# Kernel optimization log

Measured on AMD Instinct MI355X. Metric: run time of the kernel, lower is better.

Reference implementation:

```python
import jax, jax.numpy as jnp
import numpy as np

N = 200_000        # nodes
E = 2_000_000      # edges (before self loops)
D = 128            # emb_dim
L = 5              # num_layer
NUM_ATOM = 120     # num_atom_type
NUM_CHI = 3        # num_chirality_tag
NUM_BOND = 6       # num_bond_type
NUM_DIR = 3        # num_bond_direction
EPS = 1e-5


def setup_inputs() -> dict:
    key = jax.random.key(0)
    ks = jax.random.split(key, 12)
    s = 0.1
    return {
        "x": jax.random.randint(ks[0], (N, 2), 0, 3, dtype=jnp.int64) if jax.config.jax_enable_x64 else jax.random.randint(ks[0], (N, 2), 0, 3, dtype=jnp.int32),
        "edge_index": jax.random.randint(ks[1], (2, E), 0, N, dtype=jnp.int32),
        "edge_attr": jax.random.randint(ks[2], (E, 2), 0, 3, dtype=jnp.int32),
        "x_emb1": jax.random.normal(ks[3], (NUM_ATOM, D), jnp.float32) * s,
        "x_emb2": jax.random.normal(ks[4], (NUM_CHI, D), jnp.float32) * s,
        "edge_emb1": jax.random.normal(ks[5], (L, NUM_BOND, D), jnp.float32) * s,
        "edge_emb2": jax.random.normal(ks[6], (L, NUM_DIR, D), jnp.float32) * s,
        "w1": jax.random.normal(ks[7], (L, D, 2 * D), jnp.float32) * s,
        "b1": jnp.zeros((L, 2 * D), jnp.float32),
        "w2": jax.random.normal(ks[8], (L, 2 * D, D), jnp.float32) * s,
        "b2": jnp.zeros((L, D), jnp.float32),
        "bn_gamma": jnp.ones((L, D), jnp.float32),
        "bn_beta": jnp.zeros((L, D), jnp.float32),
    }


def reference(x, edge_index, edge_attr, x_emb1, x_emb2, edge_emb1, edge_emb2,
              w1, b1, w2, b2, bn_gamma, bn_beta):
    # node features: atom-type emb + chirality emb
    h = x_emb1[x[:, 0]] + x_emb2[x[:, 1]]                     # [N, D]

    # add self loops; self-loop edge_attr = [4, 0]
    loop = jnp.arange(N, dtype=edge_index.dtype)
    src = jnp.concatenate([edge_index[0], loop])              # [E+N]
    dst = jnp.concatenate([edge_index[1], loop])              # [E+N]
    ea0 = jnp.concatenate([edge_attr[:, 0], jnp.full((N,), 4, edge_attr.dtype)])
    ea1 = jnp.concatenate([edge_attr[:, 1], jnp.zeros((N,), edge_attr.dtype)])

    for l in range(L):
        e_emb = edge_emb1[l][ea0] + edge_emb2[l][ea1]         # [E+N, D]
        msg = h[src] + e_emb                                  # gather + add
        agg = jax.ops.segment_sum(msg, dst, num_segments=N)   # scatter-add
        hid = jax.nn.relu(agg @ w1[l] + b1[l])                # [N, 2D]
        hn = hid @ w2[l] + b2[l]                              # [N, D]
        # BatchNorm1d (training mode, biased variance)
        mean = hn.mean(axis=0)
        var = jnp.mean((hn - mean) ** 2, axis=0)
        hn = bn_gamma[l] * (hn - mean) * jax.lax.rsqrt(var + EPS) + bn_beta[l]
        if l < L - 1:
            hn = jax.nn.relu(hn)
        h = hn
    return h
```

## Files before the change

kernel.cpp:

```cpp
#include <hip/hip_runtime.h>

#define NN 200000
#define NPAD 200192
#define NE 2000000
#define DD 128
#define EPSF 1e-5f

typedef short short4v __attribute__((ext_vector_type(4)));
typedef short short8v __attribute__((ext_vector_type(8)));
typedef float f32x4 __attribute__((ext_vector_type(4)));
typedef unsigned long long u64;

__device__ __forceinline__ ushort f2bf(float f) {
  uint u = __float_as_uint(f);
  uint r = u + 0x7fff + ((u >> 16) & 1);
  return (ushort)(r >> 16);
}
__device__ __forceinline__ float bf2f(ushort u) { return __uint_as_float(((uint)u) << 16); }
__device__ __forceinline__ float bflo(uint v) { return __uint_as_float(v << 16); }
__device__ __forceinline__ float bfhi(uint v) { return __uint_as_float(v & 0xffff0000u); }
__device__ __forceinline__ uint packbf(float a, float b) {
  return (uint)f2bf(a) | ((uint)f2bf(b) << 16);
}

__device__ __forceinline__ short8v ldfrag(const ushort* p) {
  short4v lo = *(const short4v*)p;
  short4v hi = *(const short4v*)(p + 16);
  short8v r;
  r[0] = lo[0]; r[1] = lo[1]; r[2] = lo[2]; r[3] = lo[3];
  r[4] = hi[0]; r[5] = hi[1]; r[6] = hi[2]; r[7] = hi[3];
  return r;
}

__global__ __launch_bounds__(256) void k_init(const int* __restrict__ x,
    const float* __restrict__ e1, const float* __restrict__ e2,
    uint* __restrict__ h) {
  int t = blockIdx.x * 256 + threadIdx.x;
  if (t >= NN * 64) return;
  int node = t >> 6, cp = (t & 63) << 1;
  int a = x[2 * node], b = x[2 * node + 1];
  float2 va = *(const float2*)(e1 + (size_t)a * DD + cp);
  float2 vb = *(const float2*)(e2 + (size_t)b * DD + cp);
  h[t] = packbf(va.x + vb.x, va.y + vb.y);
}

__global__ __launch_bounds__(256) void k_cvtw(const float* __restrict__ w,
    ushort* __restrict__ wt, int K, int Nc) {
  int t = blockIdx.x * 256 + threadIdx.x;
  if (t >= 5 * K * Nc) return;
  int per = K * Nc;
  int l = t / per, r0 = t % per;
  int j = r0 & 7, lane = (r0 >> 3) & 63, idx = r0 >> 9;
  int KB = K >> 5;
  int kb = idx % KB, ct = idx / KB;
  int lr = lane & 15, qq = lane >> 4;
  int n = ct * 16 + lr;
  int k = kb * 32 + qq * 4 + (j & 3) + ((j >> 2) << 4);
  wt[t] = f2bf(w[(size_t)l * per + (size_t)k * Nc + n]);
}

__global__ __launch_bounds__(256) void k_hist(const int* __restrict__ ei,
    const int* __restrict__ ea, u64* __restrict__ hist8) {
  int e = blockIdx.x * 256 + threadIdx.x;
  if (e >= NE) return;
  int d = ei[NE + e];
  int a0 = ea[2 * e];
  int a1 = ea[2 * e + 1];
  u64 v = (1ull << (a0 * 10)) | (1ull << (30 + a1 * 10));
  atomicAdd(&hist8[(size_t)(blockIdx.x & 7) * NN + d], v);
}

__global__ __launch_bounds__(256) void k_scan1(const u64* __restrict__ hist8,
    u64* __restrict__ histsum, int* __restrict__ off, int* __restrict__ bsum) {
  __shared__ int sh[256];
  int i = blockIdx.x * 256 + threadIdx.x;
  int v = 0;
  if (i < NN) {
    u64 s = 0;
#pragma unroll
    for (int cc = 0; cc < 8; ++cc) s += hist8[(size_t)cc * NN + i];
    histsum[i] = s;
    v = (int)((s & 1023) + ((s >> 10) & 1023) + ((s >> 20) & 1023));
  }
  sh[threadIdx.x] = v;
  __syncthreads();
  for (int d = 1; d < 256; d <<= 1) {
    int xv = 0;
    if (threadIdx.x >= d) xv = sh[threadIdx.x - d];
    __syncthreads();
    if (threadIdx.x >= d) sh[threadIdx.x] += xv;
    __syncthreads();
  }
  if (i < NN) off[i] = sh[threadIdx.x] - v;
  if (threadIdx.x == 255) bsum[blockIdx.x] = sh[255];
}

__global__ __launch_bounds__(1024) void k_scan2(const int* __restrict__ bsum,
    int* __restrict__ boff, int nb) {
  __shared__ int sh[1024];
  int t = threadIdx.x;
  int v = (t < nb) ? bsum[t] : 0;
  sh[t] = v;
  __syncthreads();
  for (int d = 1; d < 1024; d <<= 1) {
    int xv = 0;
    if (t >= d) xv = sh[t - d];
    __syncthreads();
    if (t >= d) sh[t] += xv;
    __syncthreads();
  }
  if (t < nb) boff[t] = sh[t] - v;
}

__global__ __launch_bounds__(256) void k_scan3(int* __restrict__ off,
    const int* __restrict__ boff, int* __restrict__ cursor) {
  int i = blockIdx.x * 256 + threadIdx.x;
  if (i < NN) {
    int o = off[i] + boff[i >> 8];
    off[i] = o;
    cursor[i] = o;
  }
  if (i == 0) off[NN] = NE;
}

__global__ __launch_bounds__(256) void k_scatter(const int* __restrict__ ei,
    int* __restrict__ cursor, int* __restrict__ csr_src) {
  int e = blockIdx.x * 256 + threadIdx.x;
  if (e >= NE) return;
  int d = ei[NE + e];
  int p = atomicAdd(&cursor[d], 1);
  csr_src[p] = ei[e];
}

__global__ __launch_bounds__(256) void k_agg(const uint* __restrict__ h,
    uint* __restrict__ agghi, uint* __restrict__ agglo,
    const int* __restrict__ off, const int* __restrict__ src,
    const u64* __restrict__ hist,
    const float* __restrict__ E1, const float* __restrict__ E2) {
  int lane = threadIdx.x & 63;
  int node = blockIdx.x * 4 + (threadIdx.x >> 6);
  int qq = lane >> 4;
  int c = lane & 15;
  float a[8];
#pragma unroll
  for (int j = 0; j < 8; ++j) a[j] = 0.f;
  int beg = off[node], end = off[node + 1];
  int deg = end - beg;
  for (int base = 0; base < deg; base += 64) {
    int nrem = min(deg - base, 64);
    int myidx = 0;
    if (lane < nrem) myidx = src[beg + base + lane];
    int niter = (nrem + 3) >> 2;
    for (int m = 0; m < niter; m += 4) {
      int sl0 = qq + 4 * m;
      int sl1 = sl0 + 4, sl2 = sl0 + 8, sl3 = sl0 + 12;
      int s0 = __shfl(myidx, min(sl0, nrem - 1));
      int s1 = __shfl(myidx, min(sl1, nrem - 1));
      int s2 = __shfl(myidx, min(sl2, nrem - 1));
      int s3 = __shfl(myidx, min(sl3, nrem - 1));
      uint4 v0 = *(const uint4*)(h + (size_t)s0 * 64 + c * 4);
      if (sl0 < nrem) {
        a[0] += bflo(v0.x); a[1] += bfhi(v0.x);
        a[2] += bflo(v0.y); a[3] += bfhi(v0.y);
        a[4] += bflo(v0.z); a[5] += bfhi(v0.z);
        a[6] += bflo(v0.w); a[7] += bfhi(v0.w);
      }
      if (m + 1 < niter) {
        uint4 v1 = *(const uint4*)(h + (size_t)s1 * 64 + c * 4);
        if (sl1 < nrem) {
          a[0] += bflo(v1.x); a[1] += bfhi(v1.x);
          a[2] += bflo(v1.y); a[3] += bfhi(v1.y);
          a[4] += bflo(v1.z); a[5] += bfhi(v1.z);
          a[6] += bflo(v1.w); a[7] += bfhi(v1.w);
        }
      }
      if (m + 2 < niter) {
        uint4 v2 = *(const uint4*)(h + (size_t)s2 * 64 + c * 4);
        if (sl2 < nrem) {
          a[0] += bflo(v2.x); a[1] += bfhi(v2.x);
          a[2] += bflo(v2.y); a[3] += bfhi(v2.y);
          a[4] += bflo(v2.z); a[5] += bfhi(v2.z);
          a[6] += bflo(v2.w); a[7] += bfhi(v2.w);
        }
      }
      if (m + 3 < niter) {
        uint4 v3 = *(const uint4*)(h + (size_t)s3 * 64 + c * 4);
        if (sl3 < nrem) {
          a[0] += bflo(v3.x); a[1] += bfhi(v3.x);
          a[2] += bflo(v3.y); a[3] += bfhi(v3.y);
          a[4] += bflo(v3.z); a[5] += bfhi(v3.z);
          a[6] += bflo(v3.w); a[7] += bfhi(v3.w);
        }
      }
    }
  }
#pragma unroll
  for (int j = 0; j < 8; ++j) {
    a[j] += __shfl_xor(a[j], 16);
    a[j] += __shfl_xor(a[j], 32);
  }
  if (lane < 16) {
    uint4 sv = *(const uint4*)(h + (size_t)node * 64 + c * 4);
    a[0] += bflo(sv.x); a[1] += bfhi(sv.x);
    a[2] += bflo(sv.y); a[3] += bfhi(sv.y);
    a[4] += bflo(sv.z); a[5] += bfhi(sv.z);
    a[6] += bflo(sv.w); a[7] += bfhi(sv.w);
    u64 hv = hist[node];
    float cnt[7] = {
      (float)(int)(hv & 1023),
      (float)(int)((hv >> 10) & 1023),
      (float)(int)((hv >> 20) & 1023),
      1.f,
      (float)(int)((hv >> 30) & 1023) + 1.f,
      (float)(int)((hv >> 40) & 1023),
      (float)(int)((hv >> 50) & 1023)
    };
    const float* rows[7] = {E1, E1 + DD, E1 + 2 * DD, E1 + 4 * DD,
                            E2, E2 + DD, E2 + 2 * DD};
#pragma unroll
    for (int q = 0; q < 7; ++q) {
      f32x4 e0 = *(const f32x4*)(rows[q] + c * 8);
      f32x4 e1v = *(const f32x4*)(rows[q] + c * 8 + 4);
#pragma unroll
      for (int j = 0; j < 4; ++j) { a[j] += cnt[q] * e0[j]; a[4 + j] += cnt[q] * e1v[j]; }
    }
    uint4 hi4, lo4;
    {
      ushort hA, hB;
      hA = f2bf(a[0]); hB = f2bf(a[1]);
      hi4.x = (uint)hA | ((uint)hB << 16);
      lo4.x = (uint)f2bf(a[0] - bf2f(hA)) | ((uint)f2bf(a[1] - bf2f(hB)) << 16);
      hA = f2bf(a[2]); hB = f2bf(a[3]);
      hi4.y = (uint)hA | ((uint)hB << 16);
      lo4.y = (uint)f2bf(a[2] - bf2f(hA)) | ((uint)f2bf(a[3] - bf2f(hB)) << 16);
      hA = f2bf(a[4]); hB = f2bf(a[5]);
      hi4.z = (uint)hA | ((uint)hB << 16);
      lo4.z = (uint)f2bf(a[4] - bf2f(hA)) | ((uint)f2bf(a[5] - bf2f(hB)) << 16);
      hA = f2bf(a[6]); hB = f2bf(a[7]);
      hi4.w = (uint)hA | ((uint)hB << 16);
      lo4.w = (uint)f2bf(a[6] - bf2f(hA)) | ((uint)f2bf(a[7] - bf2f(hB)) << 16);
    }
    *(uint4*)(agghi + (size_t)node * 64 + c * 4) = hi4;
    *(uint4*)(agglo + (size_t)node * 64 + c * 4) = lo4;
  }
}

__global__ __launch_bounds__(512, 1) void k_mlp(
    const ushort* __restrict__ agghi, const ushort* __restrict__ agglo,
    const ushort* __restrict__ w1,
    const float* __restrict__ b1,
    const ushort* __restrict__ w2,
    const float* __restrict__ b2, float* __restrict__ hn,
    float* __restrict__ bnsums) {
  __shared__ uint4 smem4[8192];
  __shared__ float sstat[256];
  const ushort* sw1 = (const ushort*)smem4;
  const ushort* sw2 = (const ushort*)(smem4 + 4096);
  int t = threadIdx.x;
  int lane = t & 63;
  int wid = t >> 6;
  int nb = blockIdx.x * 256 + wid * 32;
  int lr = lane & 15, qq = lane >> 4;

  if (t < 256) sstat[t] = 0.f;

  short8v afh[2][4], afl[2][4];
#pragma unroll
  for (int g = 0; g < 2; ++g) {
    const ushort* ph = agghi + (size_t)(nb + g * 16 + lr) * 128 + qq * 4;
    const ushort* pl = agglo + (size_t)(nb + g * 16 + lr) * 128 + qq * 4;
#pragma unroll
    for (int kb = 0; kb < 4; ++kb) {
      afh[g][kb] = ldfrag(ph + kb * 32);
      afl[g][kb] = ldfrag(pl + kb * 32);
    }
  }

  {
    const uint4* g1 = (const uint4*)w1;
    const uint4* g2 = (const uint4*)w2;
#pragma unroll
    for (int i = 0; i < 8; ++i) smem4[i * 512 + t] = g1[i * 512 + t];
#pragma unroll
    for (int i = 0; i < 8; ++i) smem4[4096 + i * 512 + t] = g2[i * 512 + t];
  }
  __syncthreads();

  f32x4 acc2[2][8];
#pragma unroll
  for (int g = 0; g < 2; ++g)
#pragma unroll
    for (int ct = 0; ct < 8; ++ct) acc2[g][ct] = (f32x4){0.f, 0.f, 0.f, 0.f};

#pragma unroll
  for (int ph = 0; ph < 4; ++ph) {
    f32x4 acc1[2][4];
#pragma unroll
    for (int g = 0; g < 2; ++g)
#pragma unroll
      for (int ct = 0; ct < 4; ++ct) acc1[g][ct] = (f32x4){0.f, 0.f, 0.f, 0.f};
#pragma unroll
    for (int ct = 0; ct < 4; ++ct) {
      int gct = ph * 4 + ct;
#pragma unroll
      for (int kb = 0; kb < 4; ++kb) {
        short8v wf = *(const short8v*)(sw1 + ((gct * 4 + kb) * 64 + lane) * 8);
        acc1[0][ct] = __builtin_amdgcn_mfma_f32_16x16x32_bf16(wf, afh[0][kb], acc1[0][ct], 0, 0, 0);
        acc1[0][ct] = __builtin_amdgcn_mfma_f32_16x16x32_bf16(wf, afl[0][kb], acc1[0][ct], 0, 0, 0);
        acc1[1][ct] = __builtin_amdgcn_mfma_f32_16x16x32_bf16(wf, afh[1][kb], acc1[1][ct], 0, 0, 0);
        acc1[1][ct] = __builtin_amdgcn_mfma_f32_16x16x32_bf16(wf, afl[1][kb], acc1[1][ct], 0, 0, 0);
      }
    }
    short8v hfh[2][2], hfl[2][2];
#pragma unroll
    for (int i = 0; i < 2; ++i) {
      f32x4 ba = *(const f32x4*)(b1 + (ph * 4 + 2 * i) * 16 + qq * 4);
      f32x4 bb = *(const f32x4*)(b1 + (ph * 4 + 2 * i + 1) * 16 + qq * 4);
#pragma unroll
      for (int g = 0; g < 2; ++g) {
        short8v hh, hl;
#pragma unroll
        for (int r = 0; r < 4; ++r) {
          float va = fmaxf(acc1[g][2 * i][r] + ba[r], 0.f);
          float vb = fmaxf(acc1[g][2 * i + 1][r] + bb[r], 0.f);
          ushort ha = f2bf(va), hb = f2bf(vb);
          hh[r] = (short)ha; hh[4 + r] = (short)hb;
          hl[r] = (short)f2bf(va - bf2f(ha));
          hl[4 + r] = (short)f2bf(vb - bf2f(hb));
        }
        hfh[g][i] = hh; hfl[g][i] = hl;
      }
    }
#pragma unroll
    for (int ct = 0; ct < 8; ++ct) {
#pragma unroll
      for (int i = 0; i < 2; ++i) {
        int kb2 = ph * 2 + i;
        short8v wf = *(const short8v*)(sw2 + ((ct * 8 + kb2) * 64 + lane) * 8);
        acc2[0][ct] = __builtin_amdgcn_mfma_f32_16x16x32_bf16(wf, hfh[0][i], acc2[0][ct], 0, 0, 0);
        acc2[0][ct] = __builtin_amdgcn_mfma_f32_16x16x32_bf16(wf, hfl[0][i], acc2[0][ct], 0, 0, 0);
        acc2[1][ct] = __builtin_amdgcn_mfma_f32_16x16x32_bf16(wf, hfh[1][i], acc2[1][ct], 0, 0, 0);
        acc2[1][ct] = __builtin_amdgcn_mfma_f32_16x16x32_bf16(wf, hfl[1][i], acc2[1][ct], 0, 0, 0);
      }
    }
  }

  int n0 = nb + lr, n1 = nb + 16 + lr;
  float m0 = (n0 < NN) ? 1.f : 0.f;
  float m1 = (n1 < NN) ? 1.f : 0.f;
#pragma unroll
  for (int ct = 0; ct < 8; ++ct) {
    f32x4 bb = *(const f32x4*)(b2 + ct * 16 + qq * 4);
    f32x4 o0, o1;
#pragma unroll
    for (int r = 0; r < 4; ++r) {
      o0[r] = acc2[0][ct][r] + bb[r];
      o1[r] = acc2[1][ct][r] + bb[r];
    }
#pragma unroll
    for (int r = 0; r < 4; ++r) {
      float s = m0 * o0[r] + m1 * o1[r];
      float q = m0 * o0[r] * o0[r] + m1 * o1[r] * o1[r];
      s += __shfl_xor(s, 1); q += __shfl_xor(q, 1);
      s += __shfl_xor(s, 2); q += __shfl_xor(q, 2);
      s += __shfl_xor(s, 4); q += __shfl_xor(q, 4);
      s += __shfl_xor(s, 8); q += __shfl_xor(q, 8);
      if (lr == 0) {
        int col = ct * 16 + qq * 4 + r;
        atomicAdd(&sstat[col], s);
        atomicAdd(&sstat[128 + col], q);
      }
    }
    if (n0 < NN) *(f32x4*)(hn + (size_t)n0 * DD + ct * 16 + qq * 4) = o0;
    if (n1 < NN) *(f32x4*)(hn + (size_t)n1 * DD + ct * 16 + qq * 4) = o1;
  }
  __syncthreads();
  if (t < 256) atomicAdd(&bnsums[t], sstat[t]);
}

__global__ __launch_bounds__(256) void k_bnapply(const float* __restrict__ hn,
    const float* __restrict__ sums, const float* __restrict__ gamma,
    const float* __restrict__ beta, uint* __restrict__ hout,
    float* __restrict__ fout, int final_layer) {
  int t = blockIdx.x * 256 + threadIdx.x;
  if (t >= NN * 64) return;
  int node = t >> 6, cp = (t & 63) << 1;
  float2 v = *(const float2*)(hn + (size_t)node * DD + cp);
  float r[2] = {v.x, v.y};
#pragma unroll
  for (int j = 0; j < 2; ++j) {
    int col = cp + j;
    float mean = sums[col] * (1.f / NN);
    float var = sums[128 + col] * (1.f / NN) - mean * mean;
    float scale = gamma[col] * rsqrtf(var + EPSF);
    r[j] = (r[j] - mean) * scale + beta[col];
  }
  if (final_layer) {
    *(float2*)(fout + (size_t)node * DD + cp) = make_float2(r[0], r[1]);
  } else {
    hout[t] = packbf(fmaxf(r[0], 0.f), fmaxf(r[1], 0.f));
  }
}

extern "C" void kernel_launch(void* const* d_in, const int* in_sizes, int n_in,
                              void* d_out, int out_size, void* d_ws, size_t ws_size,
                              hipStream_t stream) {
  const int* x    = (const int*)d_in[0];
  const int* ei   = (const int*)d_in[1];
  const int* ea   = (const int*)d_in[2];
  const float* xe1 = (const float*)d_in[3];
  const float* xe2 = (const float*)d_in[4];
  const float* ee1 = (const float*)d_in[5];
  const float* ee2 = (const float*)d_in[6];
  const float* w1  = (const float*)d_in[7];
  const float* b1  = (const float*)d_in[8];
  const float* w2  = (const float*)d_in[9];
  const float* b2  = (const float*)d_in[10];
  const float* gam = (const float*)d_in[11];
  const float* bet = (const float*)d_in[12];
  float* out = (float*)d_out;

  char* p = (char*)d_ws;
  auto alloc = [&](size_t bytes) {
    char* r = p;
    p += (bytes + 255) & ~(size_t)255;
    return r;
  };
  uint* h      = (uint*)alloc((size_t)NN * 64 * 4);
  uint* agghi  = (uint*)alloc((size_t)NPAD * 64 * 4);
  uint* agglo  = (uint*)alloc((size_t)NPAD * 64 * 4);
  float* hn    = (float*)alloc((size_t)NPAD * DD * 4);
  ushort* w1t  = (ushort*)alloc((size_t)5 * 128 * 256 * 2);
  ushort* w2t  = (ushort*)alloc((size_t)5 * 256 * 128 * 2);
  u64* hist8   = (u64*)alloc((size_t)8 * NN * 8);
  u64* histsum = (u64*)alloc((size_t)NN * 8);
  int* csroff  = (int*)alloc((size_t)(NN + 1) * 4);
  int* cursor  = (int*)alloc((size_t)NN * 4);
  int* csrsrc  = (int*)alloc((size_t)NE * 4);
  int* bsum    = (int*)alloc(4096);
  int* boff    = (int*)alloc(4096);
  float* bnsums = (float*)alloc(5 * 1024);

  const int nscan = (NN + 255) / 256;

  hipMemsetAsync(hist8, 0, (size_t)8 * NN * 8, stream);
  hipMemsetAsync(bnsums, 0, 5 * 1024, stream);

  k_cvtw<<<(5 * 128 * 256 + 255) / 256, 256, 0, stream>>>(w1, w1t, 128, 256);
  k_cvtw<<<(5 * 256 * 128 + 255) / 256, 256, 0, stream>>>(w2, w2t, 256, 128);
  k_init<<<(NN * 64 + 255) / 256, 256, 0, stream>>>(x, xe1, xe2, h);
  k_hist<<<(NE + 255) / 256, 256, 0, stream>>>(ei, ea, hist8);
  k_scan1<<<nscan, 256, 0, stream>>>(hist8, histsum, csroff, bsum);
  k_scan2<<<1, 1024, 0, stream>>>(bsum, boff, nscan);
  k_scan3<<<nscan, 256, 0, stream>>>(csroff, boff, cursor);
  k_scatter<<<(NE + 255) / 256, 256, 0, stream>>>(ei, cursor, csrsrc);

  for (int l = 0; l < 5; ++l) {
    k_agg<<<NN / 4, 256, 0, stream>>>(h, agghi, agglo, csroff, csrsrc, histsum,
                                      ee1 + (size_t)l * 6 * DD,
                                      ee2 + (size_t)l * 3 * DD);
    k_mlp<<<NPAD / 256, 512, 0, stream>>>((const ushort*)agghi, (const ushort*)agglo,
                                          w1t + (size_t)l * 128 * 256,
                                          b1 + (size_t)l * 256,
                                          w2t + (size_t)l * 256 * 128,
                                          b2 + (size_t)l * DD, hn,
                                          bnsums + (size_t)l * 256);
    k_bnapply<<<(NN * 64 + 255) / 256, 256, 0, stream>>>(
        hn, bnsums + (size_t)l * 256, gam + (size_t)l * DD, bet + (size_t)l * DD,
        h, out, l == 4 ? 1 : 0);
  }
}
```

Measured before the change: 1.771 ms.

## Store pre-BN activations in bf16 and split scatter cursors into eight slots

The MLP kernel now writes its pre-BatchNorm output as packed bf16 instead of fp32, which halves the intermediate write and the read in the BN-apply kernel on every layer. Separately, the CSR scatter uses eight per-slot cursor arrays, indexed by block id mod 8 and seeded from the existing 8-way histogram, to reduce atomic contention on per-node cursors. The cost is extra precision loss, since BN statistics come from fp32 but the normalized values are computed from bf16-rounded data. This matters most on the final layer, which writes fp32 output. The scatter change assumes hist8's slot assignment matches blockIdx&7 in k_hist.

Result: faster. 1.692 ms (-4.5%).

```diff
diff --git a/kernel.cpp b/kernel.cpp
--- a/kernel.cpp
+++ b/kernel.cpp
@@ -113,22 +113,29 @@
 }
 
 __global__ __launch_bounds__(256) void k_scan3(int* __restrict__ off,
-    const int* __restrict__ boff, int* __restrict__ cursor) {
+    const int* __restrict__ boff, const u64* __restrict__ hist8,
+    int* __restrict__ cursor8) {
   int i = blockIdx.x * 256 + threadIdx.x;
   if (i < NN) {
     int o = off[i] + boff[i >> 8];
     off[i] = o;
-    cursor[i] = o;
+    int run = o;
+#pragma unroll
+    for (int s = 0; s < 8; ++s) {
+      cursor8[(size_t)s * NN + i] = run;
+      u64 hs = hist8[(size_t)s * NN + i];
+      run += (int)((hs & 1023) + ((hs >> 10) & 1023) + ((hs >> 20) & 1023));
+    }
   }
   if (i == 0) off[NN] = NE;
 }
 
 __global__ __launch_bounds__(256) void k_scatter(const int* __restrict__ ei,
-    int* __restrict__ cursor, int* __restrict__ csr_src) {
+    int* __restrict__ cursor8, int* __restrict__ csr_src) {
   int e = blockIdx.x * 256 + threadIdx.x;
   if (e >= NE) return;
   int d = ei[NE + e];
-  int p = atomicAdd(&cursor[d], 1);
+  int p = atomicAdd(&cursor8[(size_t)(blockIdx.x & 7) * NN + d], 1);
   csr_src[p] = ei[e];
 }
 
@@ -250,7 +257,7 @@
     const ushort* __restrict__ w1,
     const float* __restrict__ b1,
     const ushort* __restrict__ w2,
-    const float* __restrict__ b2, float* __restrict__ hn,
+    const float* __restrict__ b2, uint* __restrict__ hnb,
     float* __restrict__ bnsums) {
   __shared__ uint4 smem4[8192];
   __shared__ float sstat[256];
@@ -371,22 +378,32 @@
         atomicAdd(&sstat[128 + col], q);
       }
     }
-    if (n0 < NN) *(f32x4*)(hn + (size_t)n0 * DD + ct * 16 + qq * 4) = o0;
-    if (n1 < NN) *(f32x4*)(hn + (size_t)n1 * DD + ct * 16 + qq * 4) = o1;
+    if (n0 < NN) {
+      uint2 wv;
+      wv.x = packbf(o0[0], o0[1]);
+      wv.y = packbf(o0[2], o0[3]);
+      *(uint2*)(hnb + (size_t)n0 * 64 + ct * 8 + qq * 2) = wv;
+    }
+    if (n1 < NN) {
+      uint2 wv;
+      wv.x = packbf(o1[0], o1[1]);
+      wv.y = packbf(o1[2], o1[3]);
+      *(uint2*)(hnb + (size_t)n1 * 64 + ct * 8 + qq * 2) = wv;
+    }
   }
   __syncthreads();
   if (t < 256) atomicAdd(&bnsums[t], sstat[t]);
 }
 
-__global__ __launch_bounds__(256) void k_bnapply(const float* __restrict__ hn,
+__global__ __launch_bounds__(256) void k_bnapply(const uint* __restrict__ hnb,
     const float* __restrict__ sums, const float* __restrict__ gamma,
     const float* __restrict__ beta, uint* __restrict__ hout,
     float* __restrict__ fout, int final_layer) {
   int t = blockIdx.x * 256 + threadIdx.x;
   if (t >= NN * 64) return;
   int node = t >> 6, cp = (t & 63) << 1;
-  float2 v = *(const float2*)(hn + (size_t)node * DD + cp);
-  float r[2] = {v.x, v.y};
+  uint v = hnb[t];
+  float r[2] = {bflo(v), bfhi(v)};
 #pragma unroll
   for (int j = 0; j < 2; ++j) {
     int col = cp + j;
@@ -429,13 +446,13 @@
   uint* h      = (uint*)alloc((size_t)NN * 64 * 4);
   uint* agghi  = (uint*)alloc((size_t)NPAD * 64 * 4);
   uint* agglo  = (uint*)alloc((size_t)NPAD * 64 * 4);
-  float* hn    = (float*)alloc((size_t)NPAD * DD * 4);
+  uint* hnb    = (uint*)alloc((size_t)NPAD * 64 * 4);
   ushort* w1t  = (ushort*)alloc((size_t)5 * 128 * 256 * 2);
   ushort* w2t  = (ushort*)alloc((size_t)5 * 256 * 128 * 2);
   u64* hist8   = (u64*)alloc((size_t)8 * NN * 8);
   u64* histsum = (u64*)alloc((size_t)NN * 8);
   int* csroff  = (int*)alloc((size_t)(NN + 1) * 4);
-  int* cursor  = (int*)alloc((size_t)NN * 4);
+  int* cursor8 = (int*)alloc((size_t)8 * NN * 4);
   int* csrsrc  = (int*)alloc((size_t)NE * 4);
   int* bsum    = (int*)alloc(4096);
   int* boff    = (int*)alloc(4096);
@@ -452,8 +469,8 @@
   k_hist<<<(NE + 255) / 256, 256, 0, stream>>>(ei, ea, hist8);
   k_scan1<<<nscan, 256, 0, stream>>>(hist8, histsum, csroff, bsum);
   k_scan2<<<1, 1024, 0, stream>>>(bsum, boff, nscan);
-  k_scan3<<<nscan, 256, 0, stream>>>(csroff, boff, cursor);
-  k_scatter<<<(NE + 255) / 256, 256, 0, stream>>>(ei, cursor, csrsrc);
+  k_scan3<<<nscan, 256, 0, stream>>>(csroff, boff, hist8, cursor8);
+  k_scatter<<<(NE + 255) / 256, 256, 0, stream>>>(ei, cursor8, csrsrc);
 
   for (int l = 0; l < 5; ++l) {
     k_agg<<<NN / 4, 256, 0, stream>>>(h, agghi, agglo, csroff, csrsrc, histsum,
@@ -463,10 +480,10 @@
                                           w1t + (size_t)l * 128 * 256,
                                           b1 + (size_t)l * 256,
                                           w2t + (size_t)l * 256 * 128,
-                                          b2 + (size_t)l * DD, hn,
+                                          b2 + (size_t)l * DD, hnb,
                                           bnsums + (size_t)l * 256);
     k_bnapply<<<(NN * 64 + 255) / 256, 256, 0, stream>>>(
-        hn, bnsums + (size_t)l * 256, gam + (size_t)l * DD, bet + (size_t)l * DD,
+        hnb, bnsums + (size_t)l * 256, gam + (size_t)l * DD, bet + (size_t)l * DD,
         h, out, l == 4 ? 1 : 0);
   }
 }
```
